# Kernel optimization log

Measured on AMD Instinct MI355X. Metric: run time of the kernel, lower is better.

The kernel has to match this reference:

```python
import jax, jax.numpy as jnp
import numpy as np

HW, B, C, NH, NC, HF, WF = 2500, 2, 256, 8, 6, 64, 176
DFF = 4 * C
EPS = 1e-5

def _layernorm(x, g, b):
    m = x.mean(-1, keepdims=True)
    v = ((x - m) ** 2).mean(-1, keepdims=True)
    return (x - m) / jnp.sqrt(v + EPS) * g + b

def _mha(q, kv, in_w, in_b, ow, ob):
    # q: [L,B,C], kv: [S,B,C] (batch_first=False, torch nn.MultiheadAttention)
    L, Bq, Cq = q.shape
    S = kv.shape[0]
    Dh = Cq // NH
    qp = (q @ in_w[:Cq].T + in_b[:Cq]).reshape(L, Bq, NH, Dh)
    kp = (kv @ in_w[Cq:2 * Cq].T + in_b[Cq:2 * Cq]).reshape(S, Bq, NH, Dh)
    vp = (kv @ in_w[2 * Cq:].T + in_b[2 * Cq:]).reshape(S, Bq, NH, Dh)
    att = jnp.einsum('lbhd,sbhd->bhls', qp, kp) * (1.0 / np.sqrt(Dh))
    att = jax.nn.softmax(att, axis=-1)
    out = jnp.einsum('bhls,sbhd->lbhd', att, vp).reshape(L, Bq, Cq)
    return out @ ow.T + ob

def _grid_sample_zeros(feat, grid):
    # feat: [B,N,C,H,W], grid: [B,N,Q,2] in [-1,1]; bilinear, align_corners=False, zero padding
    Bb, N, Cc, Hf, Wf = feat.shape
    Q = grid.shape[2]
    x = (grid[..., 0] + 1.0) * (Wf / 2.0) - 0.5
    y = (grid[..., 1] + 1.0) * (Hf / 2.0) - 0.5
    x0 = jnp.floor(x); y0 = jnp.floor(y)
    wx = x - x0; wy = y - y0
    x0i = x0.astype(jnp.int32); y0i = y0.astype(jnp.int32)
    ff = feat.reshape(Bb, N, Cc, Hf * Wf)
    def corner(xi, yi, w):
        valid = (xi >= 0) & (xi < Wf) & (yi >= 0) & (yi < Hf)
        idx = jnp.clip(yi, 0, Hf - 1) * Wf + jnp.clip(xi, 0, Wf - 1)  # [B,N,Q]
        g = jnp.take_along_axis(ff, jnp.broadcast_to(idx[:, :, None, :], (Bb, N, Cc, Q)), axis=-1)
        return g * (w * valid)[:, :, None, :]
    return (corner(x0i, y0i, (1.0 - wx) * (1.0 - wy)) + corner(x0i + 1, y0i, wx * (1.0 - wy))
            + corner(x0i, y0i + 1, (1.0 - wx) * wy) + corner(x0i + 1, y0i + 1, wx * wy))

def _forward(bev_queries, prev_bev, image_feat, reference_points, camera_intrinsics, camera_extrinsics,
             in_proj_w, in_proj_b, out_proj_w, out_proj_b, tsa_norm_g, tsa_norm_b,
             sca_w, sca_b, sca_norm_g, sca_norm_b, ffn_w1, ffn_b1, ffn_w2, ffn_b2, ffn_norm_g, ffn_norm_b):
    # TSA (dropout is identity in eval)
    tsa_out = _mha(bev_queries, prev_bev, in_proj_w, in_proj_b, out_proj_w, out_proj_b)
    x = _layernorm(bev_queries + tsa_out, tsa_norm_g, tsa_norm_b)
    # SCA: ego->camera->image projection
    R = camera_extrinsics[:, :, :3, :3]            # [B,N,3,3]
    t = camera_extrinsics[:, :, :3, 3]             # [B,N,3]
    R_e2c = jnp.swapaxes(R, -1, -2)
    t_e2c = -jnp.einsum('bnij,bnj->bni', R_e2c, t)
    pts_cam = jnp.einsum('bnij,qj->bnqi', R_e2c, reference_points) + t_e2c[:, :, None, :]  # [B,N,Q,3]
    pts_img = jnp.einsum('bnij,bnqj->bnqi', camera_intrinsics, pts_cam)
    uv = pts_img[..., :2] / jnp.maximum(pts_img[..., 2:3], 1e-5)
    grid = jnp.stack([2.0 * uv[..., 0] / WF - 1.0, 2.0 * uv[..., 1] / HF - 1.0], axis=-1)  # [B,N,Q,2]
    Bq = bev_queries.shape[1]
    feat_r = image_feat.reshape(Bq, NC, C, HF, WF)
    sampled = _grid_sample_zeros(feat_r, grid).mean(axis=1)   # [B,C,Q]
    sampled = jnp.transpose(sampled, (2, 0, 1))               # [Q,B,C]
    sca_out = sampled @ sca_w.T + sca_b
    x = _layernorm(x + sca_out, sca_norm_g, sca_norm_b)
    # FFN (torch nn.GELU default = exact erf)
    h = jax.nn.gelu(x @ ffn_w1 + ffn_b1, approximate=False)
    ffn_out = h @ ffn_w2 + ffn_b2
    return _layernorm(x + ffn_out, ffn_norm_g, ffn_norm_b)

def setup_inputs():
    key = jax.random.key(0)
    ks = jax.random.split(key, 16)
    f = jnp.float32
    s = 0.02
    return {
        'bev_queries': jax.random.normal(ks[0], (HW, B, C), f),
        'prev_bev': jax.random.normal(ks[1], (HW, B, C), f),
        'image_feat': jax.random.normal(ks[2], (B * NC, C, HF, WF), f),
        'reference_points': jax.random.normal(ks[3], (HW, 3), f) * 20.0,
        'camera_intrinsics': jax.random.normal(ks[4], (B, NC, 3, 3), f),
        'camera_extrinsics': jax.random.normal(ks[5], (B, NC, 4, 4), f),
        'spatial_shapes': jnp.array([[HF, WF]], jnp.int32),
        'in_proj_w': jax.random.normal(ks[6], (3 * C, C), f) * s,
        'in_proj_b': jnp.zeros((3 * C,), f),
        'out_proj_w': jax.random.normal(ks[7], (C, C), f) * s,
        'out_proj_b': jnp.zeros((C,), f),
        'tsa_norm_g': jnp.ones((C,), f), 'tsa_norm_b': jnp.zeros((C,), f),
        'sca_w': jax.random.normal(ks[8], (C, C), f) * s,
        'sca_b': jnp.zeros((C,), f),
        'sca_norm_g': jnp.ones((C,), f), 'sca_norm_b': jnp.zeros((C,), f),
        'ffn_w1': jax.random.normal(ks[9], (C, DFF), f) * s,
        'ffn_b1': jnp.zeros((DFF,), f),
        'ffn_w2': jax.random.normal(ks[10], (DFF, C), f) * s,
        'ffn_b2': jnp.zeros((C,), f),
        'ffn_norm_g': jnp.ones((C,), f), 'ffn_norm_b': jnp.zeros((C,), f),
    }

def reference(bev_queries, prev_bev, image_feat, reference_points, camera_intrinsics, camera_extrinsics,
              in_proj_w, in_proj_b, out_proj_w, out_proj_b, tsa_norm_g, tsa_norm_b,
              sca_w, sca_b, sca_norm_g, sca_norm_b, ffn_w1, ffn_b1, ffn_w2, ffn_b2, ffn_norm_g, ffn_norm_b,
              spatial_shapes):
    return _forward(bev_queries, prev_bev, image_feat, reference_points, camera_intrinsics, camera_extrinsics,
                    in_proj_w, in_proj_b, out_proj_w, out_proj_b, tsa_norm_g, tsa_norm_b,
                    sca_w, sca_b, sca_norm_g, sca_norm_b, ffn_w1, ffn_b1, ffn_w2, ffn_b2, ffn_norm_g, ffn_norm_b)
```

## Files before the change

kernel.cpp:

```cpp
#include <hip/hip_runtime.h>

typedef unsigned short u16;
typedef __attribute__((ext_vector_type(8))) __bf16 bf8_t;
typedef __attribute__((ext_vector_type(4))) float f4_t;

union bf8u { u16 u[8]; bf8_t v; uint4 q; };

__device__ __forceinline__ float bf2f(u16 v) {
  return __uint_as_float(((unsigned int)v) << 16);
}
__device__ __forceinline__ u16 f2bf(float f) {
  union { __bf16 h; u16 u; } c;
  c.h = (__bf16)f;
  return c.u;
}
__device__ __forceinline__ float bflo(unsigned int w) { return __uint_as_float(w << 16); }
__device__ __forceinline__ float bfhi(unsigned int w) { return __uint_as_float(w & 0xFFFF0000u); }
__device__ __forceinline__ float ldf1(const void* p, size_t i, int isf32) {
  return isf32 ? ((const float*)p)[i] : bf2f(((const u16*)p)[i]);
}
__device__ __forceinline__ unsigned int cvtpk(float lo, float hi) {
  unsigned int w;
  asm("v_cvt_pk_bf16_f32 %0, %1, %2" : "=v"(w) : "v"(lo), "v"(hi));
  return w;
}

#define LQ    2500
#define LQP   2560
#define BB    2
#define CC    256
#define NCC   6
#define HFF   64
#define WFF   176
#define DFF   1024
#define MROWS 5000

#define WB_UV   256
#define WB_WQKV 240256
#define WB_WOP  633472
#define WB_WSC  764544
#define WB_WF1  895616
#define WB_WF2  1419904
#define WB_S1   1944192
#define WB_S2   (WB_S1 + 2621440)
#define WB_S3   (WB_S2 + 2621440)
#define WB_VT   (WB_S3 + 2621440)
#define WB_SB   (WB_VT + 2621440)
#define WB_H    WB_S2

__global__ void detect_k(const u16* __restrict__ rp, int* __restrict__ flag) {
  int bad = 0;
  for (int i = threadIdx.x; i < 7500; i += 64) {
    float v = bf2f(rp[i]);
    if (!(fabsf(v) < 1e6f)) bad = 1;
  }
  int anybad = __any(bad);
  if (threadIdx.x == 0) flag[0] = anybad ? 1 : 0;
}

struct WDesc {
  const void* src[3];
  u16* dst[3];
  int n[3];
};
__global__ __launch_bounds__(256) void cvtw_k(WDesc d, u16* __restrict__ vtp,
    const void* __restrict__ refp, const void* __restrict__ intr,
    const void* __restrict__ extr, float* __restrict__ uv,
    const void* __restrict__ tw1, u16* __restrict__ td1,
    const void* __restrict__ tw2, u16* __restrict__ td2,
    const int* __restrict__ flag) {
  const int df = flag[0];
  const int i = blockIdx.y;
  if (i == 5) {
    __shared__ u16 tile[64][66];
    const void* src; u16* dst; int Ks, Ns, bx;
    if (blockIdx.x < 64) { src = tw1; dst = td1; Ks = 256;  Ns = 1024; bx = blockIdx.x; }
    else                 { src = tw2; dst = td2; Ks = 1024; Ns = 256;  bx = blockIdx.x - 64; }
    const int ntn = Ns >> 6;
    const int kx = bx / ntn, nx = bx % ntn;
    const int k0 = kx * 64, n0 = nx * 64;
    const int t = threadIdx.x;
    const int col = t & 63, rq = t >> 6;
#pragma unroll
    for (int ii = 0; ii < 16; ++ii) {
      const int r = ii * 4 + rq;
      tile[col][r] = f2bf(ldf1(src, (size_t)(k0 + r) * Ns + n0 + col, df));
    }
    __syncthreads();
#pragma unroll
    for (int ii = 0; ii < 16; ++ii) {
      const int n = ii * 4 + rq;
      dst[(size_t)(n0 + n) * Ks + k0 + col] = tile[n][col];
    }
    return;
  }
  if (i == 4) {
    for (int idx = blockIdx.x * 256 + threadIdx.x; idx < BB * NCC * LQ; idx += gridDim.x * 256) {
      const int bc = idx / LQ;
      const int q = idx - bc * LQ;
      float R[3][3], tv[3], Kc[3][3], p[3];
#pragma unroll
      for (int a = 0; a < 3; ++a) {
#pragma unroll
        for (int j = 0; j < 3; ++j) {
          R[a][j] = ldf1(extr, bc*16 + a*4 + j, df);
          Kc[a][j] = ldf1(intr, bc*9 + a*3 + j, df);
        }
        tv[a] = ldf1(extr, bc*16 + a*4 + 3, df);
      }
#pragma unroll
      for (int j = 0; j < 3; ++j) p[j] = ldf1(refp, q*3 + j, df) - tv[j];
      float pc[3];
#pragma unroll
      for (int a = 0; a < 3; ++a) pc[a] = R[0][a]*p[0] + R[1][a]*p[1] + R[2][a]*p[2];
      float im[3];
#pragma unroll
      for (int a = 0; a < 3; ++a) im[a] = Kc[a][0]*pc[0] + Kc[a][1]*pc[1] + Kc[a][2]*pc[2];
      const float z = fmaxf(im[2], 1e-5f);
      uv[(size_t)idx*2 + 0] = im[0] / z - 0.5f;
      uv[(size_t)idx*2 + 1] = im[1] / z - 0.5f;
    }
    return;
  }
  if (i == 3) {
    const int n = 512 * (LQP - LQ);
    for (int j = blockIdx.x * 256 + threadIdx.x; j < n; j += gridDim.x * 256) {
      const int row = j / (LQP - LQ), col = LQ + j % (LQP - LQ);
      vtp[(size_t)row * LQP + col] = 0;
    }
    return;
  }
  const int n = d.n[i];
  for (int j = blockIdx.x * 256 + threadIdx.x; j < n; j += gridDim.x * 256) {
    if (df) {
      const float4 r = ((const float4*)d.src[i])[j];
      const unsigned int lo = (unsigned int)f2bf(r.x) | ((unsigned int)f2bf(r.y) << 16);
      const unsigned int hi = (unsigned int)f2bf(r.z) | ((unsigned int)f2bf(r.w) << 16);
      ((uint2*)d.dst[i])[j] = make_uint2(lo, hi);
    } else {
      ((uint2*)d.dst[i])[j] = ((const uint2*)d.src[i])[j];
    }
  }
}

template<int KTPL, int ACT, int NT>
__global__ __launch_bounds__(64) void gemm_nl(
    const u16* __restrict__ Xv, const u16* __restrict__ W,
    const void* __restrict__ bias,
    u16* __restrict__ Y, int M, int N, const int* __restrict__ flag)
{
  const int df = flag[0];
  const int lane = threadIdx.x;
  const int ln15 = lane & 15, l4 = lane >> 4;
  const int m0 = blockIdx.x * 32, n0 = blockIdx.y * (NT * 16);
  const int am0 = min(m0 + ln15, M - 1);
  const int am1 = min(m0 + 16 + ln15, M - 1);

  f4_t acc[2][NT];
#pragma unroll
  for (int g = 0; g < 2; ++g)
#pragma unroll
    for (int nt = 0; nt < NT; ++nt) acc[g][nt] = (f4_t){0.f, 0.f, 0.f, 0.f};

#pragma unroll 8
  for (int k0 = 0; k0 < KTPL; k0 += 32) {
    bf8u a0, a1;
    a0.q = *(const uint4*)(Xv + (size_t)am0 * KTPL + k0 + l4 * 8);
    a1.q = *(const uint4*)(Xv + (size_t)am1 * KTPL + k0 + l4 * 8);
#pragma unroll
    for (int nt = 0; nt < NT; ++nt) {
      bf8u b;
      b.q = *(const uint4*)&W[(size_t)(n0 + nt * 16 + ln15) * KTPL + k0 + l4 * 8];
      acc[0][nt] = __builtin_amdgcn_mfma_f32_16x16x32_bf16(a0.v, b.v, acc[0][nt], 0, 0, 0);
      acc[1][nt] = __builtin_amdgcn_mfma_f32_16x16x32_bf16(a1.v, b.v, acc[1][nt], 0, 0, 0);
    }
  }
#pragma unroll
  for (int g = 0; g < 2; ++g) {
#pragma unroll
    for (int nt = 0; nt < NT; ++nt) {
      const int gn = n0 + nt * 16 + ln15;
      const float bv = ldf1(bias, gn, df);
#pragma unroll
      for (int r = 0; r < 4; ++r) {
        const int gm = m0 + g * 16 + l4 * 4 + r;
        if (gm < M) {
          float x = acc[g][nt][r] + bv;
          if (ACT) x = 0.5f * x * (1.f + erff(x * 0.70710678118654752f));
          Y[(size_t)gm * N + gn] = f2bf(x);
        }
      }
    }
  }
}

template<int KT, int RES, int TOOUT>
__global__ __launch_bounds__(256) void gemm_ln(
    const u16* __restrict__ Xv, const u16* __restrict__ W,
    const void* __restrict__ bias, const void* __restrict__ resv,
    const void* __restrict__ gw, const void* __restrict__ bw,
    void* __restrict__ Yv, int M, const int* __restrict__ flag)
{
  __shared__ float sR[4][32];
  const int df = flag[0];
  const int t = threadIdx.x;
  const int lane = t & 63, wn = t >> 6;
  const int ln15 = lane & 15, l4 = lane >> 4;
  const int m0 = blockIdx.x * 32;
  const int am0 = min(m0 + ln15, M - 1);
  const int am1 = min(m0 + 16 + ln15, M - 1);

  f4_t acc[2][4];
#pragma unroll
  for (int g = 0; g < 2; ++g)
#pragma unroll
    for (int nt = 0; nt < 4; ++nt) acc[g][nt] = (f4_t){0.f, 0.f, 0.f, 0.f};

#pragma unroll 8
  for (int k0 = 0; k0 < KT; k0 += 32) {
    bf8u a0, a1;
    a0.q = *(const uint4*)(Xv + (size_t)am0 * KT + k0 + l4 * 8);
    a1.q = *(const uint4*)(Xv + (size_t)am1 * KT + k0 + l4 * 8);
#pragma unroll
    for (int nt = 0; nt < 4; ++nt) {
      bf8u b;
      b.q = *(const uint4*)&W[(size_t)(wn * 64 + nt * 16 + ln15) * KT + k0 + l4 * 8];
      acc[0][nt] = __builtin_amdgcn_mfma_f32_16x16x32_bf16(a0.v, b.v, acc[0][nt], 0, 0, 0);
      acc[1][nt] = __builtin_amdgcn_mfma_f32_16x16x32_bf16(a1.v, b.v, acc[1][nt], 0, 0, 0);
    }
  }
  float x[2][4][4];
#pragma unroll
  for (int g = 0; g < 2; ++g)
#pragma unroll
    for (int nt = 0; nt < 4; ++nt) {
      const int gn = wn * 64 + nt * 16 + ln15;
      const float bv = ldf1(bias, gn, df);
#pragma unroll
      for (int r = 0; r < 4; ++r) {
        const int gm = m0 + g * 16 + l4 * 4 + r;
        float xx = acc[g][nt][r] + bv;
        const size_t ri = (size_t)min(gm, M - 1) * CC + gn;
        if (RES == 1)      xx += bf2f(((const u16*)resv)[ri]);
        else if (RES == 2) xx += ldf1(resv, ri, df);
        x[g][nt][r] = xx;
      }
    }
#pragma unroll
  for (int g = 0; g < 2; ++g) {
    float ps[4];
#pragma unroll
    for (int r = 0; r < 4; ++r) {
      ps[r] = x[g][0][r] + x[g][1][r] + x[g][2][r] + x[g][3][r];
#pragma unroll
      for (int o = 1; o < 16; o <<= 1) ps[r] += __shfl_xor(ps[r], o);
    }
    if (ln15 == 0) {
#pragma unroll
      for (int r = 0; r < 4; ++r) sR[wn][g * 16 + l4 * 4 + r] = ps[r];
    }
  }
  __syncthreads();
  float mean[2][4];
#pragma unroll
  for (int g = 0; g < 2; ++g)
#pragma unroll
    for (int r = 0; r < 4; ++r) {
      const int row = g * 16 + l4 * 4 + r;
      mean[g][r] = (sR[0][row] + sR[1][row] + sR[2][row] + sR[3][row]) * 0.00390625f;
    }
  __syncthreads();
#pragma unroll
  for (int g = 0; g < 2; ++g) {
    float pq[4];
#pragma unroll
    for (int r = 0; r < 4; ++r) {
      float d0 = x[g][0][r] - mean[g][r], d1 = x[g][1][r] - mean[g][r];
      float d2 = x[g][2][r] - mean[g][r], d3 = x[g][3][r] - mean[g][r];
      pq[r] = d0*d0 + d1*d1 + d2*d2 + d3*d3;
#pragma unroll
      for (int o = 1; o < 16; o <<= 1) pq[r] += __shfl_xor(pq[r], o);
    }
    if (ln15 == 0) {
#pragma unroll
      for (int r = 0; r < 4; ++r) sR[wn][g * 16 + l4 * 4 + r] = pq[r];
    }
  }
  __syncthreads();
  float rstd[2][4];
#pragma unroll
  for (int g = 0; g < 2; ++g)
#pragma unroll
    for (int r = 0; r < 4; ++r) {
      const int row = g * 16 + l4 * 4 + r;
      const float v = (sR[0][row] + sR[1][row] + sR[2][row] + sR[3][row]) * 0.00390625f;
      rstd[g][r] = rsqrtf(v + 1e-5f);
    }
#pragma unroll
  for (int g = 0; g < 2; ++g)
#pragma unroll
    for (int nt = 0; nt < 4; ++nt) {
      const int gn = wn * 64 + nt * 16 + ln15;
      const float gg = ldf1(gw, gn, df);
      const float be = ldf1(bw, gn, df);
#pragma unroll
      for (int r = 0; r < 4; ++r) {
        const int gm = m0 + g * 16 + l4 * 4 + r;
        if (gm < M) {
          const float y = (x[g][nt][r] - mean[g][r]) * rstd[g][r] * gg + be;
          if (TOOUT && df) ((float*)Yv)[(size_t)gm * CC + gn] = y;
          else             ((u16*)Yv)[(size_t)gm * CC + gn] = f2bf(y);
        }
      }
    }
}

__global__ __launch_bounds__(64) void gemm_qkv(
    const void* __restrict__ Xq, const void* __restrict__ Xkv,
    const u16* __restrict__ Wqkv, const void* __restrict__ bias,
    u16* __restrict__ Qo, u16* __restrict__ Ko, u16* __restrict__ Vt,
    const int* __restrict__ flag)
{
  const int df = flag[0];
  const int lane = threadIdx.x;
  const int ln15 = lane & 15, l4 = lane >> 4;
  const int which = blockIdx.y >> 2;
  const int n0 = (blockIdx.y & 3) * 64;
  const void* Xv = (which == 0) ? Xq : Xkv;
  const u16* W = Wqkv + (size_t)which * 65536;
  const int m0 = blockIdx.x * 32;
  const int am0 = min(m0 + ln15, MROWS - 1);
  const int am1 = min(m0 + 16 + ln15, MROWS - 1);

  f4_t acc[2][4];
#pragma unroll
  for (int g = 0; g < 2; ++g)
#pragma unroll
    for (int nt = 0; nt < 4; ++nt) acc[g][nt] = (f4_t){0.f, 0.f, 0.f, 0.f};

#pragma unroll 8
  for (int k0 = 0; k0 < CC; k0 += 32) {
    bf8u a0, a1;
    if (df) {
      const float* p0 = (const float*)Xv + (size_t)am0 * CC + k0 + l4 * 8;
      float4 r0 = *(const float4*)p0, r1 = *(const float4*)(p0 + 4);
      a0.u[0]=f2bf(r0.x); a0.u[1]=f2bf(r0.y); a0.u[2]=f2bf(r0.z); a0.u[3]=f2bf(r0.w);
      a0.u[4]=f2bf(r1.x); a0.u[5]=f2bf(r1.y); a0.u[6]=f2bf(r1.z); a0.u[7]=f2bf(r1.w);
      const float* p1 = (const float*)Xv + (size_t)am1 * CC + k0 + l4 * 8;
      float4 r2 = *(const float4*)p1, r3 = *(const float4*)(p1 + 4);
      a1.u[0]=f2bf(r2.x); a1.u[1]=f2bf(r2.y); a1.u[2]=f2bf(r2.z); a1.u[3]=f2bf(r2.w);
      a1.u[4]=f2bf(r3.x); a1.u[5]=f2bf(r3.y); a1.u[6]=f2bf(r3.z); a1.u[7]=f2bf(r3.w);
    } else {
      a0.q = *(const uint4*)((const u16*)Xv + (size_t)am0 * CC + k0 + l4 * 8);
      a1.q = *(const uint4*)((const u16*)Xv + (size_t)am1 * CC + k0 + l4 * 8);
    }
#pragma unroll
    for (int nt = 0; nt < 4; ++nt) {
      bf8u b;
      b.q = *(const uint4*)&W[(size_t)(n0 + nt * 16 + ln15) * CC + k0 + l4 * 8];
      acc[0][nt] = __builtin_amdgcn_mfma_f32_16x16x32_bf16(a0.v, b.v, acc[0][nt], 0, 0, 0);
      acc[1][nt] = __builtin_amdgcn_mfma_f32_16x16x32_bf16(a1.v, b.v, acc[1][nt], 0, 0, 0);
    }
  }
#pragma unroll
  for (int g = 0; g < 2; ++g) {
#pragma unroll
    for (int nt = 0; nt < 4; ++nt) {
      const int gn = n0 + nt * 16 + ln15;
      const float bv = ldf1(bias, which * 256 + gn, df);
#pragma unroll
      for (int r = 0; r < 4; ++r) {
        const int gm = m0 + g * 16 + l4 * 4 + r;
        if (gm < MROWS) {
          const float x = acc[g][nt][r] + bv;
          if (which == 2) {
            const int tt = gm >> 1;
            const int tx = tt & 63;
            const int tp = (tx & 35) | ((tx & 12) << 1) | ((tx & 16) >> 2);
            Vt[(size_t)(gn + (gm & 1) * 256) * LQP + ((tt & ~63) | tp)] = f2bf(x);
          } else {
            u16* Y = (which == 0) ? Qo : Ko;
            Y[(size_t)gm * CC + gn] = f2bf(x);
          }
        }
      }
    }
  }
}

#define TPW 10
#define ATTN_BLOCKS (79 * 16)
__global__ __launch_bounds__(256) void attn_samp(
    const u16* __restrict__ Qw, const u16* __restrict__ Kw,
    const u16* __restrict__ Vt, u16* __restrict__ Ow,
    const void* __restrict__ feat, const float* __restrict__ uv,
    u16* __restrict__ SB, const int* __restrict__ flag)
{
  const int t = threadIdx.x;
  if (blockIdx.x >= ATTN_BLOCKS) {
    const int df = flag[0];
    const int sid = blockIdx.x - ATTN_BLOCKS;
    const int c = sid & 255;
    const int yy = sid >> 8;
    const int b = yy / 5;
    const int ch = yy % 5;
    const int qend = min((ch + 1) * 500, LQ);
    for (int q = ch * 500 + t; q < qend; q += 256) {
      float acc = 0.f;
#pragma unroll
      for (int cam = 0; cam < NCC; ++cam) {
        const int bc = b * NCC + cam;
        const float x = uv[((size_t)bc * LQ + q) * 2 + 0];
        const float y = uv[((size_t)bc * LQ + q) * 2 + 1];
        const float xf = floorf(x), yf = floorf(y);
        const int x0 = (int)xf, y0 = (int)yf;
        const float wx = x - xf, wy = y - yf;
        const size_t base = ((size_t)bc * CC + c) * (HFF * WFF);
        const bool vx0 = (x0 >= 0) & (x0 < WFF);
        const bool vx1 = (x0 + 1 >= 0) & (x0 + 1 < WFF);
        const bool vy0 = (y0 >= 0) & (y0 < HFF);
        const bool vy1 = (y0 + 1 >= 0) & (y0 + 1 < HFF);
        if (vy0) {
          const size_t rb = base + (size_t)y0 * WFF;
          if (vx0) acc += (1.f - wx) * (1.f - wy) * ldf1(feat, rb + x0, df);
          if (vx1) acc += wx * (1.f - wy) * ldf1(feat, rb + x0 + 1, df);
        }
        if (vy1) {
          const size_t rb = base + (size_t)(y0 + 1) * WFF;
          if (vx0) acc += (1.f - wx) * wy * ldf1(feat, rb + x0, df);
          if (vx1) acc += wx * wy * ldf1(feat, rb + x0 + 1, df);
        }
      }
      SB[((size_t)q * BB + b) * CC + c] = f2bf(acc * (1.f / 6.f));
    }
    return;
  }
  __shared__ float sO[4][32][33];
  __shared__ float sM[4][32];
  __shared__ float sL[4][32];
  const int lane = t & 63, w = t >> 6;
  const int ln15 = lane & 15, l4 = lane >> 4;
  const int q0 = (blockIdx.x % 79) * 32;
  const int by = blockIdx.x / 79;
  const int b = by >> 3, h = by & 7;
  const float SCL2E = 0.25505654481f;

  bf8u aqA, aqB;
  {
    const int qra = min(q0 + ln15, LQ - 1);
    const int qrb = min(q0 + 16 + ln15, LQ - 1);
    bf8u qr;
    qr.q = *(const uint4*)&Qw[((size_t)qra * BB + b) * CC + h * 32 + l4 * 8];
#pragma unroll
    for (int i = 0; i < 8; ++i) aqA.u[i] = f2bf(bf2f(qr.u[i]) * SCL2E);
    qr.q = *(const uint4*)&Qw[((size_t)qrb * BB + b) * CC + h * 32 + l4 * 8];
#pragma unroll
    for (int i = 0; i < 8; ++i) aqB.u[i] = f2bf(bf2f(qr.u[i]) * SCL2E);
  }

  f4_t oaccA[2], oaccB[2];
  oaccA[0] = (f4_t){0.f,0.f,0.f,0.f}; oaccA[1] = (f4_t){0.f,0.f,0.f,0.f};
  oaccB[0] = (f4_t){0.f,0.f,0.f,0.f}; oaccB[1] = (f4_t){0.f,0.f,0.f,0.f};
  float mA = -1e30f, lA = 0.f;
  float mB = -1e30f, lB = 0.f;

  const int kt0 = w * TPW;
  const u16* Kbase = &Kw[(size_t)b * CC + h * 32 + l4 * 8];
  const u16* Vbase = &Vt[(size_t)(by * 32 + ln15) * LQP + l4 * 8];

  bf8u bkn[4];
#pragma unroll
  for (int nt = 0; nt < 4; ++nt)
    bkn[nt].q = *(const uint4*)&Kbase[(size_t)(kt0 * 64 + nt * 16 + ln15) * CC];

  for (int kt = kt0; kt < kt0 + TPW; ++kt) {
    const int kb = kt * 64;
    bf8u av[2][2];
#pragma unroll
    for (int m = 0; m < 2; ++m)
#pragma unroll
      for (int dt = 0; dt < 2; ++dt)
        av[m][dt].q = *(const uint4*)&Vbase[(size_t)(dt * 16) * LQP + kb + m * 32];
    f4_t svA[4], svB[4];
    __builtin_amdgcn_s_setprio(1);
#pragma unroll
    for (int nt = 0; nt < 4; ++nt) {
      f4_t z = (f4_t){0.f,0.f,0.f,0.f};
      svA[nt] = __builtin_amdgcn_mfma_f32_16x16x32_bf16(bkn[nt].v, aqA.v, z, 0, 0, 0);
      f4_t z2 = (f4_t){0.f,0.f,0.f,0.f};
      svB[nt] = __builtin_amdgcn_mfma_f32_16x16x32_bf16(bkn[nt].v, aqB.v, z2, 0, 0, 0);
    }
    __builtin_amdgcn_s_setprio(0);
    if (kt + 1 < kt0 + TPW) {
#pragma unroll
      for (int nt = 0; nt < 4; ++nt)
        bkn[nt].q = *(const uint4*)&Kbase[(size_t)(kb + 64 + nt * 16 + ln15) * CC];
    }
    float pA[4][4], pB[4][4];
    if (kb + 64 <= LQ) {
#pragma unroll
      for (int nt = 0; nt < 4; ++nt)
#pragma unroll
        for (int r = 0; r < 4; ++r) { pA[nt][r] = svA[nt][r]; pB[nt][r] = svB[nt][r]; }
    } else {
#pragma unroll
      for (int nt = 0; nt < 4; ++nt)
#pragma unroll
        for (int r = 0; r < 4; ++r) {
          const bool ok = (kb + nt * 16 + l4 * 4 + r < LQ);
          pA[nt][r] = ok ? svA[nt][r] : -1e30f;
          pB[nt][r] = ok ? svB[nt][r] : -1e30f;
        }
    }
    {
      const float thr = mA + 8.f;
      bool nd = false;
#pragma unroll
      for (int nt = 0; nt < 4; ++nt)
#pragma unroll
        for (int r = 0; r < 4; ++r) nd |= (pA[nt][r] > thr);
      if (__any(nd)) {
        const float x0 = fmaxf(fmaxf(pA[0][0], pA[0][1]), fmaxf(pA[0][2], pA[0][3]));
        const float x1 = fmaxf(fmaxf(pA[1][0], pA[1][1]), fmaxf(pA[1][2], pA[1][3]));
        const float x2 = fmaxf(fmaxf(pA[2][0], pA[2][1]), fmaxf(pA[2][2], pA[2][3]));
        const float x3 = fmaxf(fmaxf(pA[3][0], pA[3][1]), fmaxf(pA[3][2], pA[3][3]));
        float mloc = fmaxf(fmaxf(x0, x1), fmaxf(x2, x3));
        mloc = fmaxf(mloc, __shfl_xor(mloc, 16));
        mloc = fmaxf(mloc, __shfl_xor(mloc, 32));
        const float mn = fmaxf(mA, mloc);
        const float alpha = __builtin_amdgcn_exp2f(mA - mn);
        mA = mn;
        lA *= alpha;
#pragma unroll
        for (int r = 0; r < 4; ++r) { oaccA[0][r] *= alpha; oaccA[1][r] *= alpha; }
      }
      float s = 0.f;
#pragma unroll
      for (int nt = 0; nt < 4; ++nt)
#pragma unroll
        for (int r = 0; r < 4; ++r) {
          const float e = __builtin_amdgcn_exp2f(pA[nt][r] - mA);
          pA[nt][r] = e; s += e;
        }
      lA += s;
    }
    {
      const float thr = mB + 8.f;
      bool nd = false;
#pragma unroll
      for (int nt = 0; nt < 4; ++nt)
#pragma unroll
        for (int r = 0; r < 4; ++r) nd |= (pB[nt][r] > thr);
      if (__any(nd)) {
        const float x0 = fmaxf(fmaxf(pB[0][0], pB[0][1]), fmaxf(pB[0][2], pB[0][3]));
        const float x1 = fmaxf(fmaxf(pB[1][0], pB[1][1]), fmaxf(pB[1][2], pB[1][3]));
        const float x2 = fmaxf(fmaxf(pB[2][0], pB[2][1]), fmaxf(pB[2][2], pB[2][3]));
        const float x3 = fmaxf(fmaxf(pB[3][0], pB[3][1]), fmaxf(pB[3][2], pB[3][3]));
        float mloc = fmaxf(fmaxf(x0, x1), fmaxf(x2, x3));
        mloc = fmaxf(mloc, __shfl_xor(mloc, 16));
        mloc = fmaxf(mloc, __shfl_xor(mloc, 32));
        const float mn = fmaxf(mB, mloc);
        const float alpha = __builtin_amdgcn_exp2f(mB - mn);
        mB = mn;
        lB *= alpha;
#pragma unroll
        for (int r = 0; r < 4; ++r) { oaccB[0][r] *= alpha; oaccB[1][r] *= alpha; }
      }
      float s = 0.f;
#pragma unroll
      for (int nt = 0; nt < 4; ++nt)
#pragma unroll
        for (int r = 0; r < 4; ++r) {
          const float e = __builtin_amdgcn_exp2f(pB[nt][r] - mB);
          pB[nt][r] = e; s += e;
        }
      lB += s;
    }
    __builtin_amdgcn_s_setprio(1);
#pragma unroll
    for (int m = 0; m < 2; ++m) {
      bf8u pba, pbb;
      pba.q = make_uint4(cvtpk(pA[2*m][0], pA[2*m][1]),   cvtpk(pA[2*m][2], pA[2*m][3]),
                         cvtpk(pA[2*m+1][0], pA[2*m+1][1]), cvtpk(pA[2*m+1][2], pA[2*m+1][3]));
      pbb.q = make_uint4(cvtpk(pB[2*m][0], pB[2*m][1]),   cvtpk(pB[2*m][2], pB[2*m][3]),
                         cvtpk(pB[2*m+1][0], pB[2*m+1][1]), cvtpk(pB[2*m+1][2], pB[2*m+1][3]));
#pragma unroll
      for (int dt = 0; dt < 2; ++dt) {
        oaccA[dt] = __builtin_amdgcn_mfma_f32_16x16x32_bf16(av[m][dt].v, pba.v, oaccA[dt], 0, 0, 0);
        oaccB[dt] = __builtin_amdgcn_mfma_f32_16x16x32_bf16(av[m][dt].v, pbb.v, oaccB[dt], 0, 0, 0);
      }
    }
    __builtin_amdgcn_s_setprio(0);
  }
  lA += __shfl_xor(lA, 16);  lA += __shfl_xor(lA, 32);
  lB += __shfl_xor(lB, 16);  lB += __shfl_xor(lB, 32);
#pragma unroll
  for (int dt = 0; dt < 2; ++dt)
#pragma unroll
    for (int r = 0; r < 4; ++r) {
      sO[w][ln15][dt * 16 + l4 * 4 + r]      = oaccA[dt][r];
      sO[w][16 + ln15][dt * 16 + l4 * 4 + r] = oaccB[dt][r];
    }
  if (l4 == 0) {
    sM[w][ln15] = mA; sL[w][ln15] = lA;
    sM[w][16 + ln15] = mB; sL[w][16 + ln15] = lB;
  }
  __syncthreads();
#pragma unroll
  for (int i = t; i < 1024; i += 256) {
    const int row = i >> 5, col = i & 31;
    const float M = fmaxf(fmaxf(sM[0][row], sM[1][row]), fmaxf(sM[2][row], sM[3][row]));
    float l = 0.f, O = 0.f;
#pragma unroll
    for (int w4 = 0; w4 < 4; ++w4) {
      const float sc = __builtin_amdgcn_exp2f(sM[w4][row] - M);
      l += sc * sL[w4][row];
      O += sc * sO[w4][row][col];
    }
    const int q = q0 + row;
    if (q < LQ)
      Ow[((size_t)q * BB + b) * CC + h * 32 + col] = f2bf(O / l);
  }
}

extern "C" void kernel_launch(void* const* d_in, const int* in_sizes, int n_in,
                              void* d_out, int out_size, void* d_ws, size_t ws_size,
                              hipStream_t stream) {
  (void)in_sizes; (void)n_in; (void)out_size; (void)ws_size;
  char* base = (char*)d_ws;
  int* flag = (int*)base;
  float* UV = (float*)(base + WB_UV);
  u16* WQKV = (u16*)(base + WB_WQKV);
  u16* WOP  = (u16*)(base + WB_WOP);
  u16* WSC  = (u16*)(base + WB_WSC);
  u16* WF1  = (u16*)(base + WB_WF1);
  u16* WF2  = (u16*)(base + WB_WF2);
  u16* S1 = (u16*)(base + WB_S1);
  u16* S2 = (u16*)(base + WB_S2);
  u16* S3 = (u16*)(base + WB_S3);
  u16* VT = (u16*)(base + WB_VT);
  u16* SB = (u16*)(base + WB_SB);
  u16* H  = (u16*)(base + WB_H);

  detect_k<<<1, 64, 0, stream>>>((const u16*)d_in[3], flag);

  WDesc wd;
  wd.src[0] = d_in[7];  wd.dst[0] = WQKV; wd.n[0] = 49152;
  wd.src[1] = d_in[9];  wd.dst[1] = WOP;  wd.n[1] = 16384;
  wd.src[2] = d_in[13]; wd.dst[2] = WSC;  wd.n[2] = 16384;
  cvtw_k<<<dim3(128, 6), 256, 0, stream>>>(wd, VT, d_in[3], d_in[4], d_in[5], UV,
                                           d_in[17], WF1, d_in[19], WF2, flag);

  gemm_qkv<<<dim3(157, 12), 64, 0, stream>>>(d_in[0], d_in[1], WQKV, d_in[8], S1, S2, VT, flag);

  attn_samp<<<ATTN_BLOCKS + 2560, 256, 0, stream>>>(S1, S2, VT, S3,
                                                    d_in[2], UV, SB, flag);

  gemm_ln<256,2,0><<<157, 256, 0, stream>>>(S3, WOP, d_in[10], d_in[0], d_in[11], d_in[12], S2, MROWS, flag);

  gemm_ln<256,1,0><<<157, 256, 0, stream>>>(SB, WSC, d_in[14], S2, d_in[15], d_in[16], S1, MROWS, flag);

  gemm_nl<256,1,4><<<dim3(157, 16), 64, 0, stream>>>(S1, WF1, d_in[18], H, MROWS, DFF, flag);
  gemm_ln<1024,1,1><<<157, 256, 0, stream>>>(H, WF2, d_in[20], S1, d_in[21], d_in[22], d_out, MROWS, flag);
}
```

Measured before the change: 465.8 us.

## Split grid sampling out of attention kernel and vectorize paired fp32 corner loads

Separates the fused attention+sampling kernel into two launches, attention alone and a standalone bilinear sampling kernel run after the output-projection GEMM. In the sampling kernel, when features are fp32 and both x corners are in range, the two horizontally adjacent texels are read with a single 8-byte load, cutting the number of gather instructions. This gives up the overlap between attention and sampling inside one launch and adds a kernel launch, in exchange for simpler per-kernel scheduling and fewer memory transactions.

```diff
diff --git a/kernel.cpp b/kernel.cpp
--- a/kernel.cpp
+++ b/kernel.cpp
@@ -24,6 +24,7 @@
   asm("v_cvt_pk_bf16_f32 %0, %1, %2" : "=v"(w) : "v"(lo), "v"(hi));
   return w;
 }
+typedef struct __attribute__((packed, aligned(4))) { float a, b; } f2u;
 
 #define LQ    2500
 #define LQP   2560
@@ -389,59 +390,18 @@
 }
 
 #define TPW 10
-#define ATTN_BLOCKS (79 * 16)
-__global__ __launch_bounds__(256) void attn_samp(
+__global__ __launch_bounds__(256) void attn_mf(
     const u16* __restrict__ Qw, const u16* __restrict__ Kw,
-    const u16* __restrict__ Vt, u16* __restrict__ Ow,
-    const void* __restrict__ feat, const float* __restrict__ uv,
-    u16* __restrict__ SB, const int* __restrict__ flag)
+    const u16* __restrict__ Vt, u16* __restrict__ Ow)
 {
-  const int t = threadIdx.x;
-  if (blockIdx.x >= ATTN_BLOCKS) {
-    const int df = flag[0];
-    const int sid = blockIdx.x - ATTN_BLOCKS;
-    const int c = sid & 255;
-    const int yy = sid >> 8;
-    const int b = yy / 5;
-    const int ch = yy % 5;
-    const int qend = min((ch + 1) * 500, LQ);
-    for (int q = ch * 500 + t; q < qend; q += 256) {
-      float acc = 0.f;
-#pragma unroll
-      for (int cam = 0; cam < NCC; ++cam) {
-        const int bc = b * NCC + cam;
-        const float x = uv[((size_t)bc * LQ + q) * 2 + 0];
-        const float y = uv[((size_t)bc * LQ + q) * 2 + 1];
-        const float xf = floorf(x), yf = floorf(y);
-        const int x0 = (int)xf, y0 = (int)yf;
-        const float wx = x - xf, wy = y - yf;
-        const size_t base = ((size_t)bc * CC + c) * (HFF * WFF);
-        const bool vx0 = (x0 >= 0) & (x0 < WFF);
-        const bool vx1 = (x0 + 1 >= 0) & (x0 + 1 < WFF);
-        const bool vy0 = (y0 >= 0) & (y0 < HFF);
-        const bool vy1 = (y0 + 1 >= 0) & (y0 + 1 < HFF);
-        if (vy0) {
-          const size_t rb = base + (size_t)y0 * WFF;
-          if (vx0) acc += (1.f - wx) * (1.f - wy) * ldf1(feat, rb + x0, df);
-          if (vx1) acc += wx * (1.f - wy) * ldf1(feat, rb + x0 + 1, df);
-        }
-        if (vy1) {
-          const size_t rb = base + (size_t)(y0 + 1) * WFF;
-          if (vx0) acc += (1.f - wx) * wy * ldf1(feat, rb + x0, df);
-          if (vx1) acc += wx * wy * ldf1(feat, rb + x0 + 1, df);
-        }
-      }
-      SB[((size_t)q * BB + b) * CC + c] = f2bf(acc * (1.f / 6.f));
-    }
-    return;
-  }
   __shared__ float sO[4][32][33];
   __shared__ float sM[4][32];
   __shared__ float sL[4][32];
+  const int t = threadIdx.x;
   const int lane = t & 63, w = t >> 6;
   const int ln15 = lane & 15, l4 = lane >> 4;
-  const int q0 = (blockIdx.x % 79) * 32;
-  const int by = blockIdx.x / 79;
+  const int q0 = blockIdx.x * 32;
+  const int by = blockIdx.y;
   const int b = by >> 3, h = by & 7;
   const float SCL2E = 0.25505654481f;
 
@@ -620,6 +580,57 @@
     const int q = q0 + row;
     if (q < LQ)
       Ow[((size_t)q * BB + b) * CC + h * 32 + col] = f2bf(O / l);
+  }
+}
+
+__global__ __launch_bounds__(256) void samp_k(
+    const void* __restrict__ feat, const float* __restrict__ uv,
+    u16* __restrict__ S, const int* __restrict__ flag)
+{
+  const int df = flag[0];
+  const int c = blockIdx.x;
+  const int b = blockIdx.y / 5;
+  const int ch = blockIdx.y % 5;
+  const int qend = min((ch + 1) * 500, LQ);
+  for (int q = ch * 500 + threadIdx.x; q < qend; q += 256) {
+    float acc = 0.f;
+#pragma unroll
+    for (int cam = 0; cam < NCC; ++cam) {
+      const int bc = b * NCC + cam;
+      const float x = uv[((size_t)bc * LQ + q) * 2 + 0];
+      const float y = uv[((size_t)bc * LQ + q) * 2 + 1];
+      const float xf = floorf(x), yf = floorf(y);
+      const int x0 = (int)xf, y0 = (int)yf;
+      const float wx = x - xf, wy = y - yf;
+      const size_t base = ((size_t)bc * CC + c) * (HFF * WFF);
+      const bool vy0 = (y0 >= 0) & (y0 < HFF);
+      const bool vy1 = (y0 + 1 >= 0) & (y0 + 1 < HFF);
+      if (df && x0 >= 0 && x0 + 1 < WFF) {
+        const float* fp = (const float*)feat + base + x0;
+        if (vy0) {
+          const f2u r0 = *(const f2u*)(fp + (size_t)y0 * WFF);
+          acc += (1.f - wy) * ((1.f - wx) * r0.a + wx * r0.b);
+        }
+        if (vy1) {
+          const f2u r1 = *(const f2u*)(fp + (size_t)(y0 + 1) * WFF);
+          acc += wy * ((1.f - wx) * r1.a + wx * r1.b);
+        }
+      } else {
+        const bool vx0 = (x0 >= 0) & (x0 < WFF);
+        const bool vx1 = (x0 + 1 >= 0) & (x0 + 1 < WFF);
+        if (vy0) {
+          const size_t rb = base + (size_t)y0 * WFF;
+          if (vx0) acc += (1.f - wx) * (1.f - wy) * ldf1(feat, rb + x0, df);
+          if (vx1) acc += wx * (1.f - wy) * ldf1(feat, rb + x0 + 1, df);
+        }
+        if (vy1) {
+          const size_t rb = base + (size_t)(y0 + 1) * WFF;
+          if (vx0) acc += (1.f - wx) * wy * ldf1(feat, rb + x0, df);
+          if (vx1) acc += wx * wy * ldf1(feat, rb + x0 + 1, df);
+        }
+      }
+    }
+    S[((size_t)q * BB + b) * CC + c] = f2bf(acc * (1.f / 6.f));
   }
 }
 
@@ -653,10 +664,11 @@
 
   gemm_qkv<<<dim3(157, 12), 64, 0, stream>>>(d_in[0], d_in[1], WQKV, d_in[8], S1, S2, VT, flag);
 
-  attn_samp<<<ATTN_BLOCKS + 2560, 256, 0, stream>>>(S1, S2, VT, S3,
-                                                    d_in[2], UV, SB, flag);
+  attn_mf<<<dim3(79, 16), 256, 0, stream>>>(S1, S2, VT, S3);
 
   gemm_ln<256,2,0><<<157, 256, 0, stream>>>(S3, WOP, d_in[10], d_in[0], d_in[11], d_in[12], S2, MROWS, flag);
+
+  samp_k<<<dim3(CC, BB * 5), 256, 0, stream>>>(d_in[2], UV, SB, flag);
 
   gemm_ln<256,1,0><<<157, 256, 0, stream>>>(SB, WSC, d_in[14], S2, d_in[15], d_in[16], S1, MROWS, flag);
 
```

Result: faster. 455.2 us (-2.3%).
